# Optimization experiments

Measured on AMD Instinct MI355X. Metric: run time of the kernel, lower is better.

The kernel has to match this reference:

```python
import jax, jax.numpy as jnp
import numpy as np

D_MODEL = 768
N_HEADS = 8
HEAD_DIM = D_MODEL // N_HEADS
D_FF = 3072
EPS = 1e-5


def _layernorm(x, g, b):
    mu = jnp.mean(x, axis=-1, keepdims=True)
    var = jnp.var(x, axis=-1, keepdims=True)
    return (x - mu) * jax.lax.rsqrt(var + EPS) * g + b


def setup_inputs() -> dict:
    key = jax.random.key(0)
    ks = jax.random.split(key, 12)
    s = 0.02
    return {
        "x": jax.random.normal(ks[0], (2, 4096, D_MODEL), dtype=jnp.float32),
        "w_qkv": jax.random.normal(ks[1], (D_MODEL, 3 * D_MODEL), dtype=jnp.float32) * s,
        "b_qkv": jnp.zeros((3 * D_MODEL,), dtype=jnp.float32),
        "w_out": jax.random.normal(ks[2], (D_MODEL, D_MODEL), dtype=jnp.float32) * s,
        "b_out": jnp.zeros((D_MODEL,), dtype=jnp.float32),
        "w_ff1": jax.random.normal(ks[3], (D_MODEL, D_FF), dtype=jnp.float32) * s,
        "b_ff1": jnp.zeros((D_FF,), dtype=jnp.float32),
        "w_ff2": jax.random.normal(ks[4], (D_FF, D_MODEL), dtype=jnp.float32) * s,
        "b_ff2": jnp.zeros((D_MODEL,), dtype=jnp.float32),
        "g1": jnp.ones((D_MODEL,), dtype=jnp.float32),
        "be1": jnp.zeros((D_MODEL,), dtype=jnp.float32),
        "g2": jnp.ones((D_MODEL,), dtype=jnp.float32),
        "be2": jnp.zeros((D_MODEL,), dtype=jnp.float32),
    }


def reference(x, w_qkv, b_qkv, w_out, b_out, w_ff1, b_ff1, w_ff2, b_ff2, g1, be1, g2, be2):
    B, S, D = x.shape
    qkv = x @ w_qkv + b_qkv  # [B,S,3D]
    q, k, v = jnp.split(qkv, 3, axis=-1)
    # [B,H,S,d]
    q = q.reshape(B, S, N_HEADS, HEAD_DIM).transpose(0, 2, 1, 3)
    k = k.reshape(B, S, N_HEADS, HEAD_DIM).transpose(0, 2, 1, 3)
    v = v.reshape(B, S, N_HEADS, HEAD_DIM).transpose(0, 2, 1, 3)
    scores = jnp.einsum("bhqd,bhkd->bhqk", q, k) / np.sqrt(HEAD_DIM).astype(np.float32)
    attn = jax.nn.softmax(scores, axis=-1)
    out = jnp.einsum("bhqk,bhkd->bhqd", attn, v)
    out = out.transpose(0, 2, 1, 3).reshape(B, S, D)
    out = out @ w_out + b_out
    x = _layernorm(x + out, g1, be1)
    h = jax.nn.gelu(x @ w_ff1 + b_ff1, approximate=False)
    ffn = h @ w_ff2 + b_ff2
    return _layernorm(x + ffn, g2, be2)
```

## Files before the change

kernel.cpp:

```cpp
#include <hip/hip_runtime.h>
#include <hip/hip_bf16.h>
#include <stdint.h>


typedef __attribute__((ext_vector_type(8))) short bf16x8;
typedef __attribute__((ext_vector_type(4))) short bf16x4;
typedef __attribute__((ext_vector_type(4))) float f32x4;

#define MFMA_BF16(a, b, c) __builtin_amdgcn_mfma_f32_16x16x32_bf16((a), (b), (c), 0, 0, 0)

#define EXP2R(x) __builtin_amdgcn_exp2f(x)

__device__ __forceinline__ short f2bs(float f) {
  return __builtin_bit_cast(short, __float2bfloat16(f));
}
__device__ __forceinline__ float bs2f(short s) {
  union { unsigned u; float f; } v;
  v.u = ((unsigned)(unsigned short)s) << 16;
  return v.f;
}

__device__ __forceinline__ void gload16(const void* g, void* l) {
  __builtin_amdgcn_global_load_lds(
      (const __attribute__((address_space(1))) unsigned int*)g,
      (__attribute__((address_space(3))) unsigned int*)l, 16, 0, 0);
}

__device__ __forceinline__ unsigned ldsoff(const void* p) {
  return (unsigned)(uintptr_t)p;
}

#define TRD(dst, base, off) \
  asm volatile("ds_read_b64_tr_b16 %0, %1 offset:" #off : "=v"(dst) : "v"(base) : "memory")

__global__ __launch_bounds__(256) void transpose_cast(const float* __restrict__ W,
                                                      short* __restrict__ Wt,
                                                      int K, int N) {
  __shared__ float tile[32][33];
  const int n0 = blockIdx.x * 32, k0 = blockIdx.y * 32;
  const int tx = threadIdx.x & 31, ty = threadIdx.x >> 5;
#pragma unroll
  for (int i = 0; i < 4; ++i)
    tile[ty + i * 8][tx] = W[(size_t)(k0 + ty + i * 8) * N + n0 + tx];
  __syncthreads();
#pragma unroll
  for (int i = 0; i < 4; ++i)
    Wt[(size_t)(n0 + ty + i * 8) * K + k0 + tx] = f2bs(tile[tx][ty + i * 8]);
}

__global__ __launch_bounds__(256) void cast_bf16(const float* __restrict__ x,
                                                 short* __restrict__ y, int n4) {
  const int i = blockIdx.x * 256 + threadIdx.x;
  if (i < n4) {
    const float4 v = *(const float4*)(x + (size_t)i * 4);
    short4 o;
    o.x = f2bs(v.x); o.y = f2bs(v.y); o.z = f2bs(v.z); o.w = f2bs(v.w);
    *(short4*)(y + (size_t)i * 4) = o;
  }
}

template <int EPI>
__global__ __launch_bounds__(256) void gemm_bt(const short* __restrict__ A,
                                               const short* __restrict__ Bt,
                                               const float* __restrict__ bias,
                                               void* __restrict__ outp,
                                               int N, int K) {
  __shared__ __align__(16) short la[3][128 * 32];
  __shared__ __align__(16) short lb[3][128 * 32];
  const int tid = threadIdx.x;
  const int lane = tid & 63, w = tid >> 6;
  const int lo = lane & 15, hi = lane >> 4;
  const int wr = w >> 1, wc = w & 1;

  const unsigned gdx = gridDim.x;
  const unsigned nwg = gdx * gridDim.y;
  unsigned lin = blockIdx.y * gdx + blockIdx.x;
  if ((nwg & 7u) == 0u) lin = (lin & 7u) * (nwg >> 3) + (lin >> 3);
  const unsigned by = lin / gdx, bx = lin - by * gdx;
  const int m0 = by * 128, n0 = bx * 128;

  f32x4 acc[4][4] = {};

  const int srow = tid >> 2;
  const int scol = (tid & 3) * 8;

  auto stage = [&](int kt, int buf) {
#pragma unroll
    for (int c = 0; c < 2; ++c) {
      gload16(A  + (size_t)(m0 + c * 64 + srow) * K + kt + scol,
              (char*)la[buf] + w * 1024 + c * 4096);
      gload16(Bt + (size_t)(n0 + c * 64 + srow) * K + kt + scol,
              (char*)lb[buf] + w * 1024 + c * 4096);
    }
  };

  const int nk = K >> 5;
  stage(0, 0);
  stage(32, 1);
  int cur = 0, nxt = 2;
  for (int t = 0; t < nk; ++t) {
    if (t + 1 < nk) asm volatile("s_waitcnt vmcnt(4)" ::: "memory");
    else            asm volatile("s_waitcnt vmcnt(0)" ::: "memory");
    __builtin_amdgcn_s_barrier();
    asm volatile("" ::: "memory");
    if (t + 2 < nk) stage((t + 2) << 5, nxt);
    bf16x8 af[4], bfr[4];
#pragma unroll
    for (int i = 0; i < 4; ++i) {
      af[i]  = *(const bf16x8*)(la[cur] + (wr * 64 + i * 16 + lo) * 32 + hi * 8);
      bfr[i] = *(const bf16x8*)(lb[cur] + (wc * 64 + i * 16 + lo) * 32 + hi * 8);
    }
#pragma unroll
    for (int mi = 0; mi < 4; ++mi)
#pragma unroll
      for (int ni = 0; ni < 4; ++ni)
        acc[mi][ni] = MFMA_BF16(af[mi], bfr[ni], acc[mi][ni]);
    cur = cur == 2 ? 0 : cur + 1;
    nxt = nxt == 2 ? 0 : nxt + 1;
  }

  const int rb = m0 + wr * 64, cb = n0 + wc * 64;
#pragma unroll
  for (int ni = 0; ni < 4; ++ni) {
    const int col = cb + ni * 16 + lo;
    const float bc = bias[col];
#pragma unroll
    for (int mi = 0; mi < 4; ++mi) {
#pragma unroll
      for (int r = 0; r < 4; ++r) {
        const int row = rb + mi * 16 + hi * 4 + r;
        const float v = acc[mi][ni][r] + bc;
        if constexpr (EPI == 0) {
          const int which = col / 768, rem = col - which * 768;
          const int hh = rem / 96, d = rem - hh * 96;
          const int bb = row >> 12, ss = row & 4095;
          ((short*)outp)[((size_t)((which * 2 + bb) * 8 + hh) * 4096 + ss) * 96 + d] = f2bs(v);
        } else if constexpr (EPI == 1) {
          ((float*)outp)[(size_t)row * N + col] = v;
        } else {
          const float ge = 0.5f * v * (1.f + erff(v * 0.70710678118654752f));
          ((short*)outp)[(size_t)row * N + col] = f2bs(ge);
        }
      }
    }
  }
}

__global__ __launch_bounds__(256, 2) void attn_fwd(const short* __restrict__ qkv,
                                                   short* __restrict__ out) {
  constexpr int SEQ = 4096;
  constexpr int NT = SEQ / 64;
  constexpr float SCALE2 = 0.10206207261596575f * 1.44269504088896f;
  constexpr float THR2 = 11.5415603f;
  const int qt = blockIdx.x, h = blockIdx.y, b = blockIdx.z;
  const int tid = threadIdx.x;
  const int lane = tid & 63, w = tid >> 6;
  const int lo = lane & 15, hi = lane >> 4;

  const size_t headsz = (size_t)SEQ * 96;
  const short* Qh = qkv + (size_t)((0 * 2 + b) * 8 + h) * headsz;
  const short* Kh = qkv + (size_t)((1 * 2 + b) * 8 + h) * headsz;
  const short* Vh = qkv + (size_t)((2 * 2 + b) * 8 + h) * headsz;

  __shared__ __align__(16) short k_lds[2][6144];
  __shared__ __align__(16) short v_lds[2][6144];
  __shared__ __align__(16) short p_lds[4][2048];

  int voff[3];
#pragma unroll
  for (int t = 0; t < 3; ++t) {
    const int c = t * 256 + tid;
    const int kq = c / 48, rem = c - kq * 48;
    const int dhi = rem >> 3, rem2 = rem & 7;
    voff[t] = (kq * 4 + (rem2 >> 1)) * 96 + dhi * 16 + (rem2 & 1) * 8;
  }

  const int qbase = qt * 128 + w * 32;
  bf16x8 qf[2][3];
#pragma unroll
  for (int f = 0; f < 2; ++f)
#pragma unroll
    for (int dk = 0; dk < 3; ++dk) {
      bf16x8 v = *(const bf16x8*)(Qh + (size_t)(qbase + f * 16 + lo) * 96 + dk * 32 + hi * 8);
#pragma unroll
      for (int i = 0; i < 8; ++i) v[i] = f2bs(bs2f(v[i]) * SCALE2);
      qf[f][dk] = v;
    }

  f32x4 o[2][6] = {};
  float mrow[2][4] = {};
  float lpart[2][4] = {};
  bool escaped = false;

  auto stage = [&](int t_next, int buf) {
    const short* Kt = Kh + (size_t)t_next * 6144;
    const short* Vt = Vh + (size_t)t_next * 6144;
    char* kd = (char*)k_lds[buf] + w * 1024;
    char* vd = (char*)v_lds[buf] + w * 1024;
#pragma unroll
    for (int t = 0; t < 3; ++t) {
      gload16((const char*)Kt + (t * 256 + tid) * 16, kd + t * 4096);
      gload16((const char*)Vt + (size_t)voff[t] * 2, vd + t * 4096);
    }
  };

  stage(0, 0);

  for (int kt = 0; kt < NT; ++kt) {
    const int cur = kt & 1;
    __syncthreads();
    if (kt + 1 < NT) stage(kt + 1, cur ^ 1);

    f32x4 s[2][4] = {};
    const short* kb = k_lds[cur];
#pragma unroll
    for (int dk = 0; dk < 3; ++dk)
#pragma unroll
      for (int c = 0; c < 4; ++c) {
        const bf16x8 kf = *(const bf16x8*)(kb + (c * 16 + lo) * 96 + dk * 32 + hi * 8);
#pragma unroll
        for (int f = 0; f < 2; ++f)
          s[f][c] = MFMA_BF16(qf[f][dk], kf, s[f][c]);
      }

    float tm = s[0][0][0];
#pragma unroll
    for (int f = 0; f < 2; ++f)
#pragma unroll
      for (int c = 0; c < 4; ++c)
#pragma unroll
        for (int r = 0; r < 4; ++r) tm = fmaxf(tm, s[f][c][r]);

    if (!__all(tm <= THR2)) {
      escaped = true;
#pragma unroll
      for (int f = 0; f < 2; ++f)
#pragma unroll
        for (int r = 0; r < 4; ++r) {
          float rm = fmaxf(fmaxf(s[f][0][r], s[f][1][r]), fmaxf(s[f][2][r], s[f][3][r]));
          rm = fmaxf(rm, __shfl_xor(rm, 1));
          rm = fmaxf(rm, __shfl_xor(rm, 2));
          rm = fmaxf(rm, __shfl_xor(rm, 4));
          rm = fmaxf(rm, __shfl_xor(rm, 8));
          const float mn = fmaxf(mrow[f][r], rm);
          const float al = EXP2R(mrow[f][r] - mn);
          mrow[f][r] = mn;
          lpart[f][r] *= al;
#pragma unroll
          for (int n = 0; n < 6; ++n) o[f][n][r] *= al;
        }
    }
    if (escaped) {
#pragma unroll
      for (int f = 0; f < 2; ++f)
#pragma unroll
        for (int c = 0; c < 4; ++c)
#pragma unroll
        for (int r = 0; r < 4; ++r) s[f][c][r] = EXP2R(s[f][c][r] - mrow[f][r]);
    } else {
#pragma unroll
      for (int f = 0; f < 2; ++f)
#pragma unroll
        for (int c = 0; c < 4; ++c)
#pragma unroll
        for (int r = 0; r < 4; ++r) s[f][c][r] = EXP2R(s[f][c][r]);
    }

    short* pw = p_lds[w];
#pragma unroll
    for (int f = 0; f < 2; ++f)
#pragma unroll
      for (int c = 0; c < 4; ++c) {
#pragma unroll
        for (int r = 0; r < 4; ++r) lpart[f][r] += s[f][c][r];
        short4 pk;
        pk.x = f2bs(s[f][c][0]);
        pk.y = f2bs(s[f][c][1]);
        pk.z = f2bs(s[f][c][2]);
        pk.w = f2bs(s[f][c][3]);
        *(short4*)(pw + (c * 4 + (lo >> 2)) * 128 + f * 64 + (lo & 3) * 16 + hi * 4) = pk;
      }

    const unsigned vb = ldsoff(v_lds[cur]) + (unsigned)(hi * 1536 + lo * 2);
    const unsigned pb = ldsoff(p_lds[w]) + (unsigned)(hi * 512 + lo * 2);

    {
      bf16x4 va[6], vbh[6], pa0[2], pa1[2];
      TRD(va[0], vb, 0);     TRD(vbh[0], vb, 768);
      TRD(va[1], vb, 128);   TRD(vbh[1], vb, 896);
      TRD(va[2], vb, 256);   TRD(vbh[2], vb, 1024);
      TRD(va[3], vb, 384);   TRD(vbh[3], vb, 1152);
      TRD(va[4], vb, 512);   TRD(vbh[4], vb, 1280);
      TRD(va[5], vb, 640);   TRD(vbh[5], vb, 1408);
      TRD(pa0[0], pb, 0);    TRD(pa1[0], pb, 256);
      TRD(pa0[1], pb, 128);  TRD(pa1[1], pb, 384);
      asm volatile("s_waitcnt lgkmcnt(0)" ::: "memory");
      __builtin_amdgcn_sched_barrier(0);
      __builtin_amdgcn_s_setprio(1);
#pragma unroll
      for (int f = 0; f < 2; ++f) {
        const bf16x8 pf = __builtin_shufflevector(pa0[f], pa1[f], 0, 1, 2, 3, 4, 5, 6, 7);
#pragma unroll
        for (int n = 0; n < 6; ++n) {
          const bf16x8 vf = __builtin_shufflevector(va[n], vbh[n], 0, 1, 2, 3, 4, 5, 6, 7);
          o[f][n] = MFMA_BF16(pf, vf, o[f][n]);
        }
      }
      __builtin_amdgcn_s_setprio(0);
    }
    {
      bf16x4 va[6], vbh[6], pa0[2], pa1[2];
      TRD(va[0], vb, 6144);  TRD(vbh[0], vb, 6912);
      TRD(va[1], vb, 6272);  TRD(vbh[1], vb, 7040);
      TRD(va[2], vb, 6400);  TRD(vbh[2], vb, 7168);
      TRD(va[3], vb, 6528);  TRD(vbh[3], vb, 7296);
      TRD(va[4], vb, 6656);  TRD(vbh[4], vb, 7424);
      TRD(va[5], vb, 6784);  TRD(vbh[5], vb, 7552);
      TRD(pa0[0], pb, 2048); TRD(pa1[0], pb, 2304);
      TRD(pa0[1], pb, 2176); TRD(pa1[1], pb, 2432);
      asm volatile("s_waitcnt lgkmcnt(0)" ::: "memory");
      __builtin_amdgcn_sched_barrier(0);
      __builtin_amdgcn_s_setprio(1);
#pragma unroll
      for (int f = 0; f < 2; ++f) {
        const bf16x8 pf = __builtin_shufflevector(pa0[f], pa1[f], 0, 1, 2, 3, 4, 5, 6, 7);
#pragma unroll
        for (int n = 0; n < 6; ++n) {
          const bf16x8 vf = __builtin_shufflevector(va[n], vbh[n], 0, 1, 2, 3, 4, 5, 6, 7);
          o[f][n] = MFMA_BF16(pf, vf, o[f][n]);
        }
      }
      __builtin_amdgcn_s_setprio(0);
    }
  }

  float inv[2][4];
#pragma unroll
  for (int f = 0; f < 2; ++f)
#pragma unroll
    for (int r = 0; r < 4; ++r) {
      float l = lpart[f][r];
      l += __shfl_xor(l, 1);
      l += __shfl_xor(l, 2);
      l += __shfl_xor(l, 4);
      l += __shfl_xor(l, 8);
      inv[f][r] = 1.f / l;
    }
#pragma unroll
  for (int f = 0; f < 2; ++f)
#pragma unroll
    for (int n = 0; n < 6; ++n)
#pragma unroll
      for (int r = 0; r < 4; ++r) {
        const int q = qbase + f * 16 + hi * 4 + r;
        out[((size_t)(b * SEQ + q)) * 768 + h * 96 + n * 16 + lo] = f2bs(o[f][n][r] * inv[f][r]);
      }
}

template <bool WB>
__global__ __launch_bounds__(192) void ln_residual(const float* __restrict__ xa,
                                                   const float* __restrict__ xr,
                                                   const float* __restrict__ g,
                                                   const float* __restrict__ be,
                                                   float* __restrict__ outf,
                                                   short* __restrict__ outb) {
  const int row = blockIdx.x, t = threadIdx.x;
  const size_t base = (size_t)row * 768 + t * 4;
  const float4 a = *(const float4*)(xa + base);
  const float4 bl = *(const float4*)(xr + base);
  const float v0 = a.x + bl.x, v1 = a.y + bl.y, v2 = a.z + bl.z, v3 = a.w + bl.w;
  float s = v0 + v1 + v2 + v3;
  float q = v0 * v0 + v1 * v1 + v2 * v2 + v3 * v3;
#pragma unroll
  for (int m = 32; m; m >>= 1) {
    s += __shfl_xor(s, m);
    q += __shfl_xor(q, m);
  }
  __shared__ float red[2][3];
  const int w = t >> 6;
  if ((t & 63) == 0) { red[0][w] = s; red[1][w] = q; }
  __syncthreads();
  s = red[0][0] + red[0][1] + red[0][2];
  q = red[1][0] + red[1][1] + red[1][2];
  const float mu = s * (1.f / 768.f);
  const float var = q * (1.f / 768.f) - mu * mu;
  const float rstd = rsqrtf(var + 1e-5f);
  const int c = t * 4;
  const float4 gg = *(const float4*)(g + c);
  const float4 bb = *(const float4*)(be + c);
  float y0 = (v0 - mu) * rstd * gg.x + bb.x;
  float y1 = (v1 - mu) * rstd * gg.y + bb.y;
  float y2 = (v2 - mu) * rstd * gg.z + bb.z;
  float y3 = (v3 - mu) * rstd * gg.w + bb.w;
  float4 ov = {y0, y1, y2, y3};
  *(float4*)(outf + base) = ov;
  if constexpr (WB) {
    short4 ob;
    ob.x = f2bs(y0); ob.y = f2bs(y1); ob.z = f2bs(y2); ob.w = f2bs(y3);
    *(short4*)(outb + base) = ob;
  }
}

extern "C" void kernel_launch(void* const* d_in, const int* in_sizes, int n_in,
                              void* d_out, int out_size, void* d_ws, size_t ws_size,
                              hipStream_t stream) {
  const float* x     = (const float*)d_in[0];
  const float* w_qkv = (const float*)d_in[1];
  const float* b_qkv = (const float*)d_in[2];
  const float* w_out = (const float*)d_in[3];
  const float* b_out = (const float*)d_in[4];
  const float* w_ff1 = (const float*)d_in[5];
  const float* b_ff1 = (const float*)d_in[6];
  const float* w_ff2 = (const float*)d_in[7];
  const float* b_ff2 = (const float*)d_in[8];
  const float* g1  = (const float*)d_in[9];
  const float* be1 = (const float*)d_in[10];
  const float* g2  = (const float*)d_in[11];
  const float* be2 = (const float*)d_in[12];

  char* ws = (char*)d_ws;
  size_t off = 0;
  auto take = [&](size_t bytes) {
    char* p = ws + off;
    off += (bytes + 255) & ~(size_t)255;
    return p;
  };
  short* wqkv_t = (short*)take((size_t)2304 * 768 * 2);
  short* wout_t = (short*)take((size_t)768 * 768 * 2);
  short* wff1_t = (short*)take((size_t)3072 * 768 * 2);
  short* wff2_t = (short*)take((size_t)768 * 3072 * 2);
  short* xb     = (short*)take((size_t)8192 * 768 * 2);
  short* qkv    = (short*)take((size_t)3 * 2 * 8 * 4096 * 96 * 2);
  short* ao     = (short*)take((size_t)8192 * 768 * 2);
  short* x1b    = (short*)take((size_t)8192 * 768 * 2);
  float* x1     = (float*)take((size_t)8192 * 768 * 4);
  if (ws_size < off) return;

  float* proj = (float*)qkv;
  short* hbuf = xb;
  float* ff2o = (float*)ao;

  cast_bf16<<<dim3(6144), dim3(256), 0, stream>>>(x, xb, 8192 * 768 / 4);
  transpose_cast<<<dim3(2304 / 32, 768 / 32), dim3(256), 0, stream>>>(w_qkv, wqkv_t, 768, 2304);
  transpose_cast<<<dim3(768 / 32, 768 / 32), dim3(256), 0, stream>>>(w_out, wout_t, 768, 768);
  transpose_cast<<<dim3(3072 / 32, 768 / 32), dim3(256), 0, stream>>>(w_ff1, wff1_t, 768, 3072);
  transpose_cast<<<dim3(768 / 32, 3072 / 32), dim3(256), 0, stream>>>(w_ff2, wff2_t, 3072, 768);

  gemm_bt<0><<<dim3(2304 / 128, 8192 / 128), dim3(256), 0, stream>>>(xb, wqkv_t, b_qkv, qkv, 2304, 768);

  attn_fwd<<<dim3(32, 8, 2), dim3(256), 0, stream>>>(qkv, ao);

  gemm_bt<1><<<dim3(768 / 128, 8192 / 128), dim3(256), 0, stream>>>(ao, wout_t, b_out, proj, 768, 768);

  ln_residual<true><<<dim3(8192), dim3(192), 0, stream>>>(x, proj, g1, be1, x1, x1b);

  gemm_bt<2><<<dim3(3072 / 128, 8192 / 128), dim3(256), 0, stream>>>(x1b, wff1_t, b_ff1, hbuf, 3072, 768);

  gemm_bt<1><<<dim3(768 / 128, 8192 / 128), dim3(256), 0, stream>>>(hbuf, wff2_t, b_ff2, ff2o, 768, 3072);

  ln_residual<false><<<dim3(8192), dim3(192), 0, stream>>>(x1, ff2o, g2, be2, (float*)d_out, nullptr);
}
```

Measured before the change: 372.7 us.

## Pad GEMM LDS rows to avoid bank conflicts and emit bf16 projection outputs

The GEMM's shared-memory staging now uses padded 80-byte rows instead of 64-byte rows, with five global-to-LDS loads per thread covering the A and B tiles. The padding targets LDS bank conflicts on fragment reads. The output-projection and FF2 GEMM epilogues now write bf16 instead of fp32, and the layernorm kernel reads them as bf16. This halves the bytes written and read between those GEMMs and the residual layernorms, at some cost in precision. The padding loads duplicate the first 8 columns into the pad slot, which spends extra load bandwidth.

After: 366.6 us. Within noise of the previous version (-1.6%).

```diff
diff --git a/kernel.cpp b/kernel.cpp
--- a/kernel.cpp
+++ b/kernel.cpp
@@ -65,8 +65,7 @@
                                                const float* __restrict__ bias,
                                                void* __restrict__ outp,
                                                int N, int K) {
-  __shared__ __align__(16) short la[3][128 * 32];
-  __shared__ __align__(16) short lb[3][128 * 32];
+  __shared__ __align__(16) short ls[3][10240];
   const int tid = threadIdx.x;
   const int lane = tid & 63, w = tid >> 6;
   const int lo = lane & 15, hi = lane >> 4;
@@ -81,17 +80,23 @@
 
   f32x4 acc[4][4] = {};
 
-  const int srow = tid >> 2;
-  const int scol = (tid & 3) * 8;
+  const short* rowsrc[5];
+#pragma unroll
+  for (int s = 0; s < 5; ++s) {
+    const int u = s * 256 + tid;
+    const int chunk = u / 320;
+    const int uin = u - chunk * 320;
+    const int r = uin / 5, ui = uin - r * 5;
+    const int koff = (ui < 4) ? ui * 8 : 0;
+    rowsrc[s] = (chunk < 2 ? A + (size_t)(m0 + chunk * 64 + r) * K
+                           : Bt + (size_t)(n0 + (chunk - 2) * 64 + r) * K) + koff;
+  }
 
   auto stage = [&](int kt, int buf) {
-#pragma unroll
-    for (int c = 0; c < 2; ++c) {
-      gload16(A  + (size_t)(m0 + c * 64 + srow) * K + kt + scol,
-              (char*)la[buf] + w * 1024 + c * 4096);
-      gload16(Bt + (size_t)(n0 + c * 64 + srow) * K + kt + scol,
-              (char*)lb[buf] + w * 1024 + c * 4096);
-    }
+    char* base = (char*)ls[buf] + w * 1024;
+#pragma unroll
+    for (int s = 0; s < 5; ++s)
+      gload16(rowsrc[s] + kt, base + s * 4096);
   };
 
   const int nk = K >> 5;
@@ -99,16 +104,17 @@
   stage(32, 1);
   int cur = 0, nxt = 2;
   for (int t = 0; t < nk; ++t) {
-    if (t + 1 < nk) asm volatile("s_waitcnt vmcnt(4)" ::: "memory");
+    if (t + 1 < nk) asm volatile("s_waitcnt vmcnt(5)" ::: "memory");
     else            asm volatile("s_waitcnt vmcnt(0)" ::: "memory");
     __builtin_amdgcn_s_barrier();
     asm volatile("" ::: "memory");
     if (t + 2 < nk) stage((t + 2) << 5, nxt);
     bf16x8 af[4], bfr[4];
+    const char* lbase = (const char*)ls[cur];
 #pragma unroll
     for (int i = 0; i < 4; ++i) {
-      af[i]  = *(const bf16x8*)(la[cur] + (wr * 64 + i * 16 + lo) * 32 + hi * 8);
-      bfr[i] = *(const bf16x8*)(lb[cur] + (wc * 64 + i * 16 + lo) * 32 + hi * 8);
+      af[i]  = *(const bf16x8*)(lbase + (wr * 64 + i * 16 + lo) * 80 + hi * 16);
+      bfr[i] = *(const bf16x8*)(lbase + 10240 + (wc * 64 + i * 16 + lo) * 80 + hi * 16);
     }
 #pragma unroll
     for (int mi = 0; mi < 4; ++mi)
@@ -136,7 +142,7 @@
           const int bb = row >> 12, ss = row & 4095;
           ((short*)outp)[((size_t)((which * 2 + bb) * 8 + hh) * 4096 + ss) * 96 + d] = f2bs(v);
         } else if constexpr (EPI == 1) {
-          ((float*)outp)[(size_t)row * N + col] = v;
+          ((short*)outp)[(size_t)row * N + col] = f2bs(v);
         } else {
           const float ge = 0.5f * v * (1.f + erff(v * 0.70710678118654752f));
           ((short*)outp)[(size_t)row * N + col] = f2bs(ge);
@@ -359,7 +365,7 @@
 
 template <bool WB>
 __global__ __launch_bounds__(192) void ln_residual(const float* __restrict__ xa,
-                                                   const float* __restrict__ xr,
+                                                   const short* __restrict__ xr,
                                                    const float* __restrict__ g,
                                                    const float* __restrict__ be,
                                                    float* __restrict__ outf,
@@ -367,8 +373,9 @@
   const int row = blockIdx.x, t = threadIdx.x;
   const size_t base = (size_t)row * 768 + t * 4;
   const float4 a = *(const float4*)(xa + base);
-  const float4 bl = *(const float4*)(xr + base);
-  const float v0 = a.x + bl.x, v1 = a.y + bl.y, v2 = a.z + bl.z, v3 = a.w + bl.w;
+  const short4 bl = *(const short4*)(xr + base);
+  const float v0 = a.x + bs2f(bl.x), v1 = a.y + bs2f(bl.y);
+  const float v2 = a.z + bs2f(bl.z), v3 = a.w + bs2f(bl.w);
   float s = v0 + v1 + v2 + v3;
   float q = v0 * v0 + v1 * v1 + v2 * v2 + v3 * v3;
 #pragma unroll
@@ -436,9 +443,9 @@
   float* x1     = (float*)take((size_t)8192 * 768 * 4);
   if (ws_size < off) return;
 
-  float* proj = (float*)qkv;
+  short* proj = qkv;
   short* hbuf = xb;
-  float* ff2o = (float*)ao;
+  short* ff2o = ao;
 
   cast_bf16<<<dim3(6144), dim3(256), 0, stream>>>(x, xb, 8192 * 768 / 4);
   transpose_cast<<<dim3(2304 / 32, 768 / 32), dim3(256), 0, stream>>>(w_qkv, wqkv_t, 768, 2304);
```
